# Performance work log

Hardware: AMD Instinct MI355X
Metric: run time of the kernel (lower is better)

Reference implementation:

```python
import jax, jax.numpy as jnp
import numpy as np

B, S, HID = 2, 4096, 2048
NH, NKV, HD = 32, 8, 64
GROUPS = NH // NKV
ROPE_THETA = 10000.0


def _rope_cos_sin(seq_len, dim, dtype):
    inv_freq = 1.0 / (ROPE_THETA ** (jnp.arange(0, dim, 2, dtype=jnp.float32) / dim))
    pos = jnp.arange(seq_len, dtype=jnp.float32)
    freqs = pos[:, None] * inv_freq[None, :]          # [S, D/2]
    emb = jnp.concatenate([freqs, freqs], axis=-1)    # [S, D]
    return jnp.cos(emb).astype(dtype), jnp.sin(emb).astype(dtype)


def _rotate_half(x):
    x1, x2 = jnp.split(x, 2, axis=-1)
    return jnp.concatenate([-x2, x1], axis=-1)


def _apply_rope(x, cos, sin):
    # x: [B, H, S, D]; cos/sin: [S, D]
    return x * cos[None, None] + _rotate_half(x) * sin[None, None]


def kappa(x):
    return jax.nn.elu(x) + 1.0


def setup_inputs() -> dict:
    key = jax.random.key(0)
    ks = jax.random.split(key, 6)
    sc = 0.02
    return {
        "hidden_states": jax.random.normal(ks[0], (B, S, HID), jnp.float32),
        "Wq": jax.random.normal(ks[1], (HID, NH * HD), jnp.float32) * sc,
        "Wk": jax.random.normal(ks[2], (HID, NKV * HD), jnp.float32) * sc,
        "Wv": jax.random.normal(ks[3], (HID, NKV * HD), jnp.float32) * sc,
        "Wphi": jax.random.normal(ks[4], (HID, HID), jnp.float32) * sc,
        "Wo": jax.random.normal(ks[5], (HID, HID), jnp.float32) * sc,
    }


def reference(hidden_states, Wq, Wk, Wv, Wphi, Wo):
    bsz, q_len, _ = hidden_states.shape

    q = (hidden_states @ Wq).reshape(bsz, q_len, NH, HD).transpose(0, 2, 1, 3)   # [B,NH,S,D]
    k = (hidden_states @ Wk).reshape(bsz, q_len, NKV, HD).transpose(0, 2, 1, 3)  # [B,NKV,S,D]
    v = (hidden_states @ Wv).reshape(bsz, q_len, NKV, HD).transpose(0, 2, 1, 3)

    cos, sin = _rope_cos_sin(q_len, HD, hidden_states.dtype)
    q = _apply_rope(q, cos, sin)
    k = _apply_rope(k, cos, sin)

    # repeat_kv for GQA: [B,NKV,S,D] -> [B,NH,S,D]
    k = jnp.repeat(k, GROUPS, axis=1)
    v = jnp.repeat(v, GROUPS, axis=1)

    Qk = kappa(q)   # [B,NH,S,D]
    Kk = kappa(k)

    Qg = Qk.mean(axis=2)                                # [B,NH,D] global query
    logits = jnp.einsum("bnd,bnsd->bns", Qg, Kk)        # [B,NH,S]
    alpha = jax.nn.softmax(logits, axis=-1) * float(q_len)

    # KV aggregation: [B,NH,D,D] state
    outer_sum = jnp.einsum("bns,bnsd,bnsf->bndf", alpha, Kk, v)
    result_attn = jnp.einsum("bnsd,bndf->bnsf", Qk, outer_sum)  # [B,NH,S,D]

    X_phi = (hidden_states @ Wphi).reshape(bsz, q_len, NH, HD).transpose(0, 2, 1, 3)
    ctx = (X_phi * result_attn).transpose(0, 2, 1, 3).reshape(bsz, q_len, HID)
    return ctx @ Wo
```

## Files before the change

### kernel.cpp

```cpp
#include <hip/hip_runtime.h>
#include <hip/hip_bf16.h>

#define B_ 2
#define S_ 4096
#define HID_ 2048
#define NH_ 32
#define NKV_ 8
#define HD_ 64
#define GROUPS_ 4
#define NCH_ 32
#define NLIN_ 5120

typedef short short8 __attribute__((ext_vector_type(8)));
typedef float floatx4 __attribute__((ext_vector_type(4)));

__device__ __forceinline__ float bf2f(unsigned short u){
  union { unsigned int i; float f; } v; v.i = ((unsigned int)u) << 16; return v.f;
}
__device__ __forceinline__ unsigned short f2bf(float f){
  union { float f; unsigned int i; } v; v.f = f;
  unsigned int i = v.i;
  unsigned int r = (i + 0x7fffu + ((i >> 16) & 1u)) >> 16;
  return (unsigned short)r;
}

__device__ __forceinline__ void async_copy16(unsigned short* lds, const unsigned short* g){
  __builtin_amdgcn_global_load_lds((const __attribute__((address_space(1))) void*)g,
                                   (__attribute__((address_space(3))) void*)lds,
                                   16, 0, 0);
}

__global__ void conv_bf16(const float* __restrict__ x, unsigned short* __restrict__ y, int n4){
  int i = blockIdx.x * 256 + threadIdx.x;
  if (i < n4){
    float4 v = ((const float4*)x)[i];
    ushort4 o;
    o.x = f2bf(v.x); o.y = f2bf(v.y); o.z = f2bf(v.z); o.w = f2bf(v.w);
    ((ushort4*)y)[i] = o;
  }
}

__global__ void transpose_all(const float* __restrict__ Wq, const float* __restrict__ Wk,
                              const float* __restrict__ Wv, const float* __restrict__ Wphi,
                              const float* __restrict__ Wo,
                              unsigned short* __restrict__ wcat, unsigned short* __restrict__ wot){
  const float* W; unsigned short* Wt; int N;
  switch (blockIdx.z){
    case 0:  W = Wq;   Wt = wcat;                              N = 2048; break;
    case 1:  W = Wk;   Wt = wcat + (size_t)2048 * HID_;        N = 512;  break;
    case 2:  W = Wv;   Wt = wcat + (size_t)2560 * HID_;        N = 512;  break;
    case 3:  W = Wphi; Wt = wcat + (size_t)3072 * HID_;        N = 2048; break;
    default: W = Wo;   Wt = wot;                               N = 2048; break;
  }
  int n0 = blockIdx.x * 32, k0 = blockIdx.y * 32;
  if (n0 >= N) return;
  __shared__ float tile[32][33];
  int tx = threadIdx.x, ty = threadIdx.y;
  #pragma unroll
  for (int j = 0; j < 4; j++)
    tile[ty + j*8][tx] = W[(size_t)(k0 + ty + j*8) * N + n0 + tx];
  __syncthreads();
  #pragma unroll
  for (int j = 0; j < 4; j++)
    Wt[(size_t)(n0 + ty + j*8) * HID_ + k0 + tx] = f2bf(tile[tx][ty + j*8]);
}

#define GTILE 16384

__global__ __launch_bounds__(512, 2) void gemm256(
    const unsigned short* __restrict__ A, const unsigned short* __restrict__ Bt,
    void* __restrict__ Cv, int M, int N, int K, int cbf16)
{
  __shared__ __align__(16) unsigned short As[2 * GTILE];
  __shared__ __align__(16) unsigned short Bs[2 * GTILE];

  const int tid = threadIdx.x;
  const int w = tid >> 6, lane = tid & 63;
  const int wr = w >> 2, wc = w & 3;
  const int l15 = lane & 15, quad = lane >> 4;

  const int nbx = N >> 8;
  int flat = blockIdx.y * nbx + blockIdx.x;
  int nwg  = nbx * (M >> 8);
  int cpx  = nwg >> 3;
  int swz  = (flat & 7) * cpx + (flat >> 3);
  int bx = swz % nbx, by = swz / nbx;
  const int m0 = by << 8, n0 = bx << 8;

  const int srow = (w << 3) + (lane >> 3);
  const int scc  = (lane & 7) ^ (lane >> 3);
  const unsigned short* gA = A  + (size_t)(m0 + srow) * K + scc * 8;
  const unsigned short* gB = Bt + (size_t)(n0 + srow) * K + scc * 8;
  const size_t rs64  = (size_t)64  * K;
  const size_t rs128 = (size_t)128 * K;
  unsigned short* lA0 = As + (w << 9);
  unsigned short* lB0 = Bs + (w << 9);

#define STAGE_A(bsel, h, t) do { \
    unsigned short* _d = lA0 + (bsel) * GTILE + (h) * 8192; \
    const unsigned short* _g = gA + (size_t)(h) * rs128 + (size_t)(t) * 64; \
    async_copy16(_d, _g); \
    async_copy16(_d + 4096, _g + rs64); \
  } while (0)
#define STAGE_B(bsel, h, t) do { \
    unsigned short* _d = lB0 + (bsel) * GTILE + (h) * 8192; \
    const unsigned short* _g = gB + (size_t)(h) * rs128 + (size_t)(t) * 64; \
    async_copy16(_d, _g); \
    async_copy16(_d + 4096, _g + rs64); \
  } while (0)
#define SCHED0 __builtin_amdgcn_sched_barrier(0)

  const int ks0  = ((quad     ^ (lane & 7)) << 3);
  const int ks1  = (((4+quad) ^ (lane & 7)) << 3);
  const int arow0 = (wr * 64 + l15) * 64;
  const int brow0 = (wc * 32 + l15) * 64;

  floatx4 acc[8][4] = {};
  short8 af[8][2], bfr[4][2];

  const int nt = K >> 6;

  STAGE_A(0, 0, 0); STAGE_A(0, 1, 0); STAGE_B(0, 0, 0); STAGE_B(0, 1, 0);
  if (nt > 1){
    STAGE_A(1, 0, 1); STAGE_B(1, 0, 1); STAGE_B(1, 1, 1);
    asm volatile("s_waitcnt vmcnt(6)" ::: "memory");
  } else {
    asm volatile("s_waitcnt vmcnt(0)" ::: "memory");
  }
  SCHED0;
  __builtin_amdgcn_s_barrier();
  SCHED0;

  for (int T = 0; T < nt; ++T){
    const int cb = T & 1;
    const unsigned short* Ab = As + cb * GTILE;
    const unsigned short* Bb = Bs + cb * GTILE;

    #pragma unroll
    for (int m = 0; m < 4; ++m){
      af[m][0] = *(const short8*)(Ab + arow0 + m * 1024 + ks0);
      af[m][1] = *(const short8*)(Ab + arow0 + m * 1024 + ks1);
    }
    #pragma unroll
    for (int n = 0; n < 2; ++n){
      bfr[n][0] = *(const short8*)(Bb + brow0 + n * 1024 + ks0);
      bfr[n][1] = *(const short8*)(Bb + brow0 + n * 1024 + ks1);
    }
    if (T + 1 < nt){ STAGE_A(cb ^ 1, 1, T + 1); }
    SCHED0; __builtin_amdgcn_s_barrier(); SCHED0;
    __builtin_amdgcn_s_setprio(1);
    #pragma unroll
    for (int k = 0; k < 2; ++k)
      #pragma unroll
      for (int m = 0; m < 4; ++m)
        #pragma unroll
        for (int n = 0; n < 2; ++n)
          acc[m][n] = __builtin_amdgcn_mfma_f32_16x16x32_bf16(af[m][k], bfr[n][k], acc[m][n], 0, 0, 0);
    __builtin_amdgcn_s_setprio(0);
    SCHED0; __builtin_amdgcn_s_barrier(); SCHED0;

    #pragma unroll
    for (int n = 2; n < 4; ++n){
      bfr[n][0] = *(const short8*)(Bb + brow0 + 8192 + (n - 2) * 1024 + ks0);
      bfr[n][1] = *(const short8*)(Bb + brow0 + 8192 + (n - 2) * 1024 + ks1);
    }
    if (T + 2 < nt){ STAGE_A(cb, 0, T + 2); }
    SCHED0; __builtin_amdgcn_s_barrier(); SCHED0;
    __builtin_amdgcn_s_setprio(1);
    #pragma unroll
    for (int k = 0; k < 2; ++k)
      #pragma unroll
      for (int m = 0; m < 4; ++m)
        #pragma unroll
        for (int n = 2; n < 4; ++n)
          acc[m][n] = __builtin_amdgcn_mfma_f32_16x16x32_bf16(af[m][k], bfr[n][k], acc[m][n], 0, 0, 0);
    __builtin_amdgcn_s_setprio(0);
    SCHED0; __builtin_amdgcn_s_barrier(); SCHED0;

    #pragma unroll
    for (int m = 4; m < 8; ++m){
      af[m][0] = *(const short8*)(Ab + arow0 + 8192 + (m - 4) * 1024 + ks0);
      af[m][1] = *(const short8*)(Ab + arow0 + 8192 + (m - 4) * 1024 + ks1);
    }
    if (T + 2 < nt){ STAGE_B(cb, 0, T + 2); }
    SCHED0; __builtin_amdgcn_s_barrier(); SCHED0;
    __builtin_amdgcn_s_setprio(1);
    #pragma unroll
    for (int k = 0; k < 2; ++k)
      #pragma unroll
      for (int m = 4; m < 8; ++m)
        #pragma unroll
        for (int n = 0; n < 2; ++n)
          acc[m][n] = __builtin_amdgcn_mfma_f32_16x16x32_bf16(af[m][k], bfr[n][k], acc[m][n], 0, 0, 0);
    __builtin_amdgcn_s_setprio(0);
    SCHED0; __builtin_amdgcn_s_barrier(); SCHED0;

    if (T + 2 < nt){
      STAGE_B(cb, 1, T + 2);
      asm volatile("s_waitcnt vmcnt(6)" ::: "memory");
    } else {
      asm volatile("s_waitcnt vmcnt(0)" ::: "memory");
    }
    SCHED0; __builtin_amdgcn_s_barrier(); SCHED0;
    __builtin_amdgcn_s_setprio(1);
    #pragma unroll
    for (int k = 0; k < 2; ++k)
      #pragma unroll
      for (int m = 4; m < 8; ++m)
        #pragma unroll
        for (int n = 2; n < 4; ++n)
          acc[m][n] = __builtin_amdgcn_mfma_f32_16x16x32_bf16(af[m][k], bfr[n][k], acc[m][n], 0, 0, 0);
    __builtin_amdgcn_s_setprio(0);
    SCHED0; __builtin_amdgcn_s_barrier(); SCHED0;
  }

#undef STAGE_A
#undef STAGE_B
#undef SCHED0

  if (cbf16){
    unsigned short* Cb = (unsigned short*)Cv;
    #pragma unroll
    for (int mi = 0; mi < 8; ++mi){
      const int row = m0 + (mi & 3) * 16 + wr * 64 + (mi >> 2) * 128 + quad * 4;
      #pragma unroll
      for (int ni = 0; ni < 4; ++ni){
        const int col = n0 + (ni & 1) * 16 + wc * 32 + (ni >> 1) * 128 + l15;
        #pragma unroll
        for (int r = 0; r < 4; ++r)
          Cb[(size_t)(row + r) * N + col] = f2bf(acc[mi][ni][r]);
      }
    }
  } else {
    float* Cf = (float*)Cv;
    #pragma unroll
    for (int mi = 0; mi < 8; ++mi){
      const int row = m0 + (mi & 3) * 16 + wr * 64 + (mi >> 2) * 128 + quad * 4;
      #pragma unroll
      for (int ni = 0; ni < 4; ++ni){
        const int col = n0 + (ni & 1) * 16 + wc * 32 + (ni >> 1) * 128 + l15;
        #pragma unroll
        for (int r = 0; r < 4; ++r)
          Cf[(size_t)(row + r) * N + col] = acc[mi][ni][r];
      }
    }
  }
}

__global__ void rope_fused(const unsigned short* __restrict__ lin,
                           unsigned short* __restrict__ Qk, unsigned short* __restrict__ Kk){
  int blk = blockIdx.x;
  if (blk < 32768){
    int idx = blk * 256 + threadIdx.x;
    int i = idx & 31;
    int n = (idx >> 5) & (NH_ - 1);
    int s = (idx >> 10) & (S_ - 1);
    int b = idx >> 22;
    float invf = exp2f(-(float)i * (13.287712379549449f / 32.0f));
    float ang = (float)s * invf;
    float c = cosf(ang), sn = sinf(ang);
    size_t in_o = (size_t)(b * S_ + s) * NLIN_ + n * HD_;
    float x1 = bf2f(lin[in_o + i]);
    float x2 = bf2f(lin[in_o + i + 32]);
    float r1 = x1 * c - x2 * sn;
    float r2 = x2 * c + x1 * sn;
    r1 = r1 > 0.f ? r1 + 1.f : __expf(r1);
    r2 = r2 > 0.f ? r2 + 1.f : __expf(r2);
    size_t o = ((size_t)(b * NH_ + n) * S_ + s) * HD_;
    Qk[o + i] = f2bf(r1);
    Qk[o + i + 32] = f2bf(r2);
  } else {
    int idx = (blk - 32768) * 256 + threadIdx.x;
    int i = idx & 31;
    int kv = (idx >> 5) & (NKV_ - 1);
    int s = (idx >> 8) & (S_ - 1);
    int b = idx >> 20;
    float invf = exp2f(-(float)i * (13.287712379549449f / 32.0f));
    float ang = (float)s * invf;
    float c = cosf(ang), sn = sinf(ang);
    size_t in_o = (size_t)(b * S_ + s) * NLIN_ + 2048 + kv * HD_;
    float x1 = bf2f(lin[in_o + i]);
    float x2 = bf2f(lin[in_o + i + 32]);
    float r1 = x1 * c - x2 * sn;
    float r2 = x2 * c + x1 * sn;
    r1 = r1 > 0.f ? r1 + 1.f : __expf(r1);
    r2 = r2 > 0.f ? r2 + 1.f : __expf(r2);
    size_t o = ((size_t)(b * NKV_ + kv) * S_ + s) * HD_;
    Kk[o + i] = f2bf(r1);
    Kk[o + i + 32] = f2bf(r2);
  }
}

__global__ __launch_bounds__(256) void qg_mean(const unsigned short* __restrict__ Qk,
                                               float* __restrict__ Qg){
  int bn = blockIdx.x, chunk = blockIdx.y;
  int tid = threadIdx.x;
  int dgrp = tid & 7, sgrp = tid >> 3;
  const unsigned short* base = Qk + (size_t)bn * S_ * HD_
                             + (size_t)(chunk * 256 + sgrp) * HD_ + dgrp * 8;
  float acc[8] = {};
  #pragma unroll
  for (int i = 0; i < 8; i++){
    short8 v = *(const short8*)(base + (size_t)i * 32 * HD_);
    #pragma unroll
    for (int e = 0; e < 8; e++) acc[e] += bf2f((unsigned short)v[e]);
  }
  __shared__ float red[256][8];
  #pragma unroll
  for (int e = 0; e < 8; e++) red[tid][e] = acc[e];
  __syncthreads();
  if (tid < 64){
    int dg = tid >> 3, e = tid & 7;
    float s = 0.f;
    #pragma unroll
    for (int g = 0; g < 32; g++) s += red[g * 8 + dg][e];
    atomicAdd(&Qg[bn * 64 + tid], s * (1.0f / (float)S_));
  }
}

__global__ __launch_bounds__(256) void logits_kernel(const unsigned short* __restrict__ Kk,
                                                     const float* __restrict__ Qg,
                                                     float* __restrict__ logits){
  int bn = blockIdx.x, chunk = blockIdx.y;
  int b = bn / NH_, n = bn % NH_, kv = n / GROUPS_;
  int tid = threadIdx.x;
  __shared__ float qg[64];
  if (tid < 64) qg[tid] = Qg[bn * 64 + tid];
  __syncthreads();
  int s = chunk * 256 + tid;
  const unsigned short* row = Kk + ((size_t)(b * NKV_ + kv) * S_ + s) * HD_;
  float acc = 0.f;
  #pragma unroll
  for (int c = 0; c < 8; c++){
    short8 v = *(const short8*)(row + c * 8);
    #pragma unroll
    for (int e = 0; e < 8; e++) acc += qg[c * 8 + e] * bf2f((unsigned short)v[e]);
  }
  logits[(size_t)bn * S_ + s] = acc;
}

__global__ __launch_bounds__(256) void softmax_kernel(const float* __restrict__ logits,
                                                      float* __restrict__ alpha){
  int bn = blockIdx.x;
  int tid = threadIdx.x;
  float l[16];
  float mymax = -1e30f;
  #pragma unroll
  for (int j = 0; j < 16; j++){
    l[j] = logits[(size_t)bn * S_ + j * 256 + tid];
    mymax = fmaxf(mymax, l[j]);
  }
  __shared__ float red[256];
  red[tid] = mymax; __syncthreads();
  for (int st = 128; st > 0; st >>= 1){
    if (tid < st) red[tid] = fmaxf(red[tid], red[tid + st]);
    __syncthreads();
  }
  float gmax = red[0];
  __syncthreads();
  float mysum = 0.f;
  #pragma unroll
  for (int j = 0; j < 16; j++){ l[j] = __expf(l[j] - gmax); mysum += l[j]; }
  red[tid] = mysum; __syncthreads();
  for (int st = 128; st > 0; st >>= 1){
    if (tid < st) red[tid] += red[tid + st];
    __syncthreads();
  }
  float inv = (float)S_ / red[0];
  #pragma unroll
  for (int j = 0; j < 16; j++)
    alpha[(size_t)bn * S_ + j * 256 + tid] = l[j] * inv;
}

__global__ __launch_bounds__(256) void outer_sum_kernel(const unsigned short* __restrict__ Kk,
                                                        const unsigned short* __restrict__ lin,
                                                        const float* __restrict__ alpha,
                                                        float* __restrict__ part){
  int bkv = blockIdx.x, chunk = blockIdx.y;
  int b = bkv >> 3, kv = bkv & 7;
  int tid = threadIdx.x;
  int d = tid >> 2, fb = (tid & 3) * 16;
  __shared__ float ks[64][64];
  __shared__ float vs[64][64];
  __shared__ float as4[64][4];
  float acc[4][16] = {};
  const unsigned short* kb = Kk + (size_t)(b * NKV_ + kv) * S_ * HD_;
  const int SPC = S_ / NCH_;

  for (int t = 0; t < SPC / 64; t++){
    int ss = chunk * SPC + t * 64;
    #pragma unroll
    for (int jj = 0; jj < 4; jj++){
      int idx4 = jj * 256 + tid;
      int si = idx4 >> 4, c4 = (idx4 & 15) * 4;
      ushort4 kv4 = *(const ushort4*)(kb + (size_t)(ss + si) * HD_ + c4);
      ks[si][c4]   = bf2f(kv4.x); ks[si][c4+1] = bf2f(kv4.y);
      ks[si][c4+2] = bf2f(kv4.z); ks[si][c4+3] = bf2f(kv4.w);
      ushort4 vv4 = *(const ushort4*)(lin + (size_t)(b * S_ + ss + si) * NLIN_ + 2560 + kv * HD_ + c4);
      vs[si][c4]   = bf2f(vv4.x); vs[si][c4+1] = bf2f(vv4.y);
      vs[si][c4+2] = bf2f(vv4.z); vs[si][c4+3] = bf2f(vv4.w);
    }
    {
      int si = tid >> 2, h = tid & 3;
      as4[si][h] = alpha[(size_t)(b * NH_ + kv * GROUPS_ + h) * S_ + ss + si];
    }
    __syncthreads();
    #pragma unroll 4
    for (int si = 0; si < 64; si++){
      float k = ks[si][d];
      float4 a4 = *(const float4*)&as4[si][0];
      float4 v0 = *(const float4*)&vs[si][fb];
      float4 v1 = *(const float4*)&vs[si][fb + 4];
      float4 v2 = *(const float4*)&vs[si][fb + 8];
      float4 v3 = *(const float4*)&vs[si][fb + 12];
      float ak0 = a4.x * k, ak1 = a4.y * k, ak2 = a4.z * k, ak3 = a4.w * k;
      acc[0][0]  += ak0 * v0.x; acc[0][1]  += ak0 * v0.y; acc[0][2]  += ak0 * v0.z; acc[0][3]  += ak0 * v0.w;
      acc[0][4]  += ak0 * v1.x; acc[0][5]  += ak0 * v1.y; acc[0][6]  += ak0 * v1.z; acc[0][7]  += ak0 * v1.w;
      acc[0][8]  += ak0 * v2.x; acc[0][9]  += ak0 * v2.y; acc[0][10] += ak0 * v2.z; acc[0][11] += ak0 * v2.w;
      acc[0][12] += ak0 * v3.x; acc[0][13] += ak0 * v3.y; acc[0][14] += ak0 * v3.z; acc[0][15] += ak0 * v3.w;
      acc[1][0]  += ak1 * v0.x; acc[1][1]  += ak1 * v0.y; acc[1][2]  += ak1 * v0.z; acc[1][3]  += ak1 * v0.w;
      acc[1][4]  += ak1 * v1.x; acc[1][5]  += ak1 * v1.y; acc[1][6]  += ak1 * v1.z; acc[1][7]  += ak1 * v1.w;
      acc[1][8]  += ak1 * v2.x; acc[1][9]  += ak1 * v2.y; acc[1][10] += ak1 * v2.z; acc[1][11] += ak1 * v2.w;
      acc[1][12] += ak1 * v3.x; acc[1][13] += ak1 * v3.y; acc[1][14] += ak1 * v3.z; acc[1][15] += ak1 * v3.w;
      acc[2][0]  += ak2 * v0.x; acc[2][1]  += ak2 * v0.y; acc[2][2]  += ak2 * v0.z; acc[2][3]  += ak2 * v0.w;
      acc[2][4]  += ak2 * v1.x; acc[2][5]  += ak2 * v1.y; acc[2][6]  += ak2 * v1.z; acc[2][7]  += ak2 * v1.w;
      acc[2][8]  += ak2 * v2.x; acc[2][9]  += ak2 * v2.y; acc[2][10] += ak2 * v2.z; acc[2][11] += ak2 * v2.w;
      acc[2][12] += ak2 * v3.x; acc[2][13] += ak2 * v3.y; acc[2][14] += ak2 * v3.z; acc[2][15] += ak2 * v3.w;
      acc[3][0]  += ak3 * v0.x; acc[3][1]  += ak3 * v0.y; acc[3][2]  += ak3 * v0.z; acc[3][3]  += ak3 * v0.w;
      acc[3][4]  += ak3 * v1.x; acc[3][5]  += ak3 * v1.y; acc[3][6]  += ak3 * v1.z; acc[3][7]  += ak3 * v1.w;
      acc[3][8]  += ak3 * v2.x; acc[3][9]  += ak3 * v2.y; acc[3][10] += ak3 * v2.z; acc[3][11] += ak3 * v2.w;
      acc[3][12] += ak3 * v3.x; acc[3][13] += ak3 * v3.y; acc[3][14] += ak3 * v3.z; acc[3][15] += ak3 * v3.w;
    }
    __syncthreads();
  }

  #pragma unroll
  for (int h = 0; h < 4; h++){
    float* pb = part + ((size_t)(chunk * 16 + bkv) * 4 + h) * 4096 + d * 64 + fb;
    #pragma unroll
    for (int j = 0; j < 4; j++)
      *(float4*)&pb[j * 4] = *(float4*)&acc[h][j * 4];
  }
}

__global__ __launch_bounds__(256) void osum_reduce_t(const float* __restrict__ part,
                                                     unsigned short* __restrict__ osumb){
  int bn = blockIdx.x;
  int tid = threadIdx.x;
  __shared__ float os[64][65];
  const float4* p4 = (const float4*)part;
  #pragma unroll
  for (int r = 0; r < 4; r++){
    int idx4 = r * 256 + tid;
    float4 s = {0.f, 0.f, 0.f, 0.f};
    #pragma unroll 8
    for (int c = 0; c < NCH_; c++){
      float4 v = p4[(size_t)c * 65536 + bn * 1024 + idx4];
      s.x += v.x; s.y += v.y; s.z += v.z; s.w += v.w;
    }
    int d = idx4 >> 4;
    int f0 = (idx4 & 15) * 4;
    os[d][f0] = s.x; os[d][f0+1] = s.y; os[d][f0+2] = s.z; os[d][f0+3] = s.w;
  }
  __syncthreads();
  int f = tid >> 2, d0 = (tid & 3) * 16;
  unsigned short hi[16], lo[16];
  #pragma unroll
  for (int j = 0; j < 16; j++){
    float x = os[d0 + j][f];
    unsigned short h = f2bf(x);
    hi[j] = h;
    lo[j] = f2bf(x - bf2f(h));
  }
  unsigned short* oh = osumb + ((size_t)bn * 2) * 4096 + (size_t)f * 64 + d0;
  unsigned short* ol = oh + 4096;
  *(short8*)(oh)     = *(const short8*)(hi);
  *(short8*)(oh + 8) = *(const short8*)(hi + 8);
  *(short8*)(ol)     = *(const short8*)(lo);
  *(short8*)(ol + 8) = *(const short8*)(lo + 8);
}

__global__ __launch_bounds__(256) void ctx_mfma(const unsigned short* __restrict__ Qk,
                                                const unsigned short* __restrict__ osumb,
                                                const unsigned short* __restrict__ lin,
                                                unsigned short* __restrict__ ctx){
  int bn = blockIdx.x, sc = blockIdx.y;
  int b = bn >> 5, n = bn & 31;
  int tid = threadIdx.x;
  int w = tid >> 6, lane = tid & 63;
  int l15 = lane & 15, quad = lane >> 4;

  const unsigned short* obase = osumb + ((size_t)bn * 2) * 4096;
  short8 bh[4][2], bl[4][2];
  #pragma unroll
  for (int nf = 0; nf < 4; nf++){
    int f = nf * 16 + l15;
    #pragma unroll
    for (int kh = 0; kh < 2; kh++){
      bh[nf][kh] = *(const short8*)(obase + (size_t)f * 64 + kh * 32 + quad * 8);
      bl[nf][kh] = *(const short8*)(obase + 4096 + (size_t)f * 64 + kh * 32 + quad * 8);
    }
  }

  int s0 = sc * 256 + w * 64;
  const unsigned short* qbase = Qk + ((size_t)bn * S_ + s0) * HD_;
  floatx4 acc[4][4] = {};
  #pragma unroll
  for (int m = 0; m < 4; m++){
    short8 a0 = *(const short8*)(qbase + (size_t)(m * 16 + l15) * HD_ + quad * 8);
    short8 a1 = *(const short8*)(qbase + (size_t)(m * 16 + l15) * HD_ + 32 + quad * 8);
    #pragma unroll
    for (int nf = 0; nf < 4; nf++){
      acc[m][nf] = __builtin_amdgcn_mfma_f32_16x16x32_bf16(a0, bh[nf][0], acc[m][nf], 0, 0, 0);
      acc[m][nf] = __builtin_amdgcn_mfma_f32_16x16x32_bf16(a1, bh[nf][1], acc[m][nf], 0, 0, 0);
      acc[m][nf] = __builtin_amdgcn_mfma_f32_16x16x32_bf16(a0, bl[nf][0], acc[m][nf], 0, 0, 0);
      acc[m][nf] = __builtin_amdgcn_mfma_f32_16x16x32_bf16(a1, bl[nf][1], acc[m][nf], 0, 0, 0);
    }
  }

  #pragma unroll
  for (int m = 0; m < 4; m++){
    #pragma unroll
    for (int r = 0; r < 4; r++){
      int s = s0 + m * 16 + quad * 4 + r;
      const unsigned short* xp = lin + (size_t)(b * S_ + s) * NLIN_ + 3072 + n * HD_;
      unsigned short* cp = ctx + (size_t)(b * S_ + s) * HID_ + n * HD_;
      #pragma unroll
      for (int nf = 0; nf < 4; nf++){
        int f = nf * 16 + l15;
        cp[f] = f2bf(bf2f(xp[f]) * acc[m][nf][r]);
      }
    }
  }
}

extern "C" void kernel_launch(void* const* d_in, const int* in_sizes, int n_in,
                              void* d_out, int out_size, void* d_ws, size_t ws_size,
                              hipStream_t stream) {
  const float* hs   = (const float*)d_in[0];
  const float* Wq   = (const float*)d_in[1];
  const float* Wk   = (const float*)d_in[2];
  const float* Wv   = (const float*)d_in[3];
  const float* Wphi = (const float*)d_in[4];
  const float* Wo   = (const float*)d_in[5];
  float* out = (float*)d_out;

  char* ws = (char*)d_ws;
  const size_t M = (size_t)B_ * S_;
  size_t off = 0;
  auto alloc = [&](size_t bytes){ size_t o = off; off += (bytes + 255) & ~(size_t)255; return o; };

  size_t off_x     = alloc(M * HID_ * 4);
  size_t off_wcat  = alloc((size_t)NLIN_ * HID_ * 2);
  size_t off_wot   = alloc((size_t)HID_ * HID_ * 2);
  size_t off_lin   = alloc(M * NLIN_ * 2);
  size_t off_qk    = alloc(M * HID_ * 2);
  size_t off_kk    = alloc(M * 512 * 2);
  size_t off_qg    = alloc(64 * 64 * 4);
  size_t off_alph  = alloc((size_t)B_ * NH_ * S_ * 4);
  size_t off_osumb = alloc((size_t)64 * 2 * 4096 * 2);
  (void)ws_size;

  unsigned short* hsb  = (unsigned short*)(ws + off_x);
  float*          part = (float*)(ws + off_x);
  unsigned short* ctx  = (unsigned short*)(ws + off_x);
  unsigned short* wcat = (unsigned short*)(ws + off_wcat);
  unsigned short* wot  = (unsigned short*)(ws + off_wot);
  unsigned short* lin  = (unsigned short*)(ws + off_lin);
  unsigned short* qk = (unsigned short*)(ws + off_qk);
  unsigned short* kk = (unsigned short*)(ws + off_kk);
  float* qg   = (float*)(ws + off_qg);
  float* alph = (float*)(ws + off_alph);
  unsigned short* osumb = (unsigned short*)(ws + off_osumb);

  conv_bf16<<<(int)(M * HID_ / 4 / 256), 256, 0, stream>>>(hs, hsb, (int)(M * HID_ / 4));
  transpose_all<<<dim3(64, 64, 5), dim3(32, 8), 0, stream>>>(Wq, Wk, Wv, Wphi, Wo, wcat, wot);
  gemm256<<<dim3(NLIN_/256, M/256), 512, 0, stream>>>(hsb, wcat, lin, (int)M, NLIN_, HID_, 1);
  rope_fused<<<32768 + 8192, 256, 0, stream>>>(lin, qk, kk);
  hipMemsetAsync(qg, 0, 64 * 64 * 4, stream);
  qg_mean<<<dim3(B_ * NH_, S_ / 256), 256, 0, stream>>>(qk, qg);
  logits_kernel<<<dim3(B_ * NH_, S_ / 256), 256, 0, stream>>>(kk, qg, alph);
  softmax_kernel<<<B_ * NH_, 256, 0, stream>>>(alph, alph);
  outer_sum_kernel<<<dim3(B_ * NKV_, NCH_), 256, 0, stream>>>(kk, lin, alph, part);
  osum_reduce_t<<<64, 256, 0, stream>>>(part, osumb);
  ctx_mfma<<<dim3(B_ * NH_, S_ / 64 / 4), 256, 0, stream>>>(qk, osumb, lin, ctx);
  gemm256<<<dim3(HID_/256, M/256), 512, 0, stream>>>(ctx, wot, out, (int)M, HID_, HID_, 0);
}
```

Before: 516.6 us.

## Fuse query mean into RoPE kernel and stage ctx epilogue through shared memory

The RoPE/kappa kernel now accumulates the per-head query mean while writing Qk, which removes the separate qg_mean pass that re-read all of Qk. Each block handles 256 sequence positions per head and uses fast __sincosf. The ctx_mfma epilogue writes accumulators to LDS as bf16, then performs coalesced 16-byte loads of X_phi and 16-byte stores of ctx in place of scattered 2-byte accesses. The risks are fewer, longer-running blocks in the RoPE kernel (1280 blocks in place of about 41k), an extra bf16 rounding of the attention result before the multiply, and the lower accuracy of __sincosf at large angles.

Measured after the change: 515.5 us. Within noise of the previous version (-0.2%).

```diff
diff --git a/kernel.cpp b/kernel.cpp
--- a/kernel.cpp
+++ b/kernel.cpp
@@ -247,74 +247,60 @@
   }
 }
 
-__global__ void rope_fused(const unsigned short* __restrict__ lin,
-                           unsigned short* __restrict__ Qk, unsigned short* __restrict__ Kk){
-  int blk = blockIdx.x;
-  if (blk < 32768){
-    int idx = blk * 256 + threadIdx.x;
-    int i = idx & 31;
-    int n = (idx >> 5) & (NH_ - 1);
-    int s = (idx >> 10) & (S_ - 1);
-    int b = idx >> 22;
-    float invf = exp2f(-(float)i * (13.287712379549449f / 32.0f));
-    float ang = (float)s * invf;
-    float c = cosf(ang), sn = sinf(ang);
-    size_t in_o = (size_t)(b * S_ + s) * NLIN_ + n * HD_;
-    float x1 = bf2f(lin[in_o + i]);
-    float x2 = bf2f(lin[in_o + i + 32]);
-    float r1 = x1 * c - x2 * sn;
-    float r2 = x2 * c + x1 * sn;
-    r1 = r1 > 0.f ? r1 + 1.f : __expf(r1);
-    r2 = r2 > 0.f ? r2 + 1.f : __expf(r2);
-    size_t o = ((size_t)(b * NH_ + n) * S_ + s) * HD_;
-    Qk[o + i] = f2bf(r1);
-    Qk[o + i + 32] = f2bf(r2);
+__global__ __launch_bounds__(256) void rope_fused(const unsigned short* __restrict__ lin,
+                                                  unsigned short* __restrict__ Qk,
+                                                  unsigned short* __restrict__ Kk,
+                                                  float* __restrict__ Qg){
+  int bx = blockIdx.x, sc = blockIdx.y;
+  int tid = threadIdx.x;
+  int i = tid & 31, si = tid >> 5;
+  float invf = exp2f(-(float)i * (13.287712379549449f / 32.0f));
+  if (bx < 64){
+    int bn = bx, b = bx >> 5, n = bx & 31;
+    float qa0 = 0.f, qa1 = 0.f;
+    for (int j = 0; j < 32; ++j){
+      int s = sc * 256 + j * 8 + si;
+      size_t in_o = (size_t)(b * S_ + s) * NLIN_ + n * HD_;
+      float x1 = bf2f(lin[in_o + i]);
+      float x2 = bf2f(lin[in_o + i + 32]);
+      float sn, c;
+      __sincosf((float)s * invf, &sn, &c);
+      float r1 = x1 * c - x2 * sn;
+      float r2 = x2 * c + x1 * sn;
+      r1 = r1 > 0.f ? r1 + 1.f : __expf(r1);
+      r2 = r2 > 0.f ? r2 + 1.f : __expf(r2);
+      size_t o = ((size_t)bn * S_ + s) * HD_;
+      Qk[o + i] = f2bf(r1);
+      Qk[o + i + 32] = f2bf(r2);
+      qa0 += r1; qa1 += r2;
+    }
+    __shared__ float red[8][64];
+    red[si][i] = qa0;
+    red[si][i + 32] = qa1;
+    __syncthreads();
+    if (tid < 64){
+      float ssum = 0.f;
+      #pragma unroll
+      for (int g = 0; g < 8; ++g) ssum += red[g][tid];
+      atomicAdd(&Qg[bn * 64 + tid], ssum * (1.0f / (float)S_));
+    }
   } else {
-    int idx = (blk - 32768) * 256 + threadIdx.x;
-    int i = idx & 31;
-    int kv = (idx >> 5) & (NKV_ - 1);
-    int s = (idx >> 8) & (S_ - 1);
-    int b = idx >> 20;
-    float invf = exp2f(-(float)i * (13.287712379549449f / 32.0f));
-    float ang = (float)s * invf;
-    float c = cosf(ang), sn = sinf(ang);
-    size_t in_o = (size_t)(b * S_ + s) * NLIN_ + 2048 + kv * HD_;
-    float x1 = bf2f(lin[in_o + i]);
-    float x2 = bf2f(lin[in_o + i + 32]);
-    float r1 = x1 * c - x2 * sn;
-    float r2 = x2 * c + x1 * sn;
-    r1 = r1 > 0.f ? r1 + 1.f : __expf(r1);
-    r2 = r2 > 0.f ? r2 + 1.f : __expf(r2);
-    size_t o = ((size_t)(b * NKV_ + kv) * S_ + s) * HD_;
-    Kk[o + i] = f2bf(r1);
-    Kk[o + i + 32] = f2bf(r2);
-  }
-}
-
-__global__ __launch_bounds__(256) void qg_mean(const unsigned short* __restrict__ Qk,
-                                               float* __restrict__ Qg){
-  int bn = blockIdx.x, chunk = blockIdx.y;
-  int tid = threadIdx.x;
-  int dgrp = tid & 7, sgrp = tid >> 3;
-  const unsigned short* base = Qk + (size_t)bn * S_ * HD_
-                             + (size_t)(chunk * 256 + sgrp) * HD_ + dgrp * 8;
-  float acc[8] = {};
-  #pragma unroll
-  for (int i = 0; i < 8; i++){
-    short8 v = *(const short8*)(base + (size_t)i * 32 * HD_);
-    #pragma unroll
-    for (int e = 0; e < 8; e++) acc[e] += bf2f((unsigned short)v[e]);
-  }
-  __shared__ float red[256][8];
-  #pragma unroll
-  for (int e = 0; e < 8; e++) red[tid][e] = acc[e];
-  __syncthreads();
-  if (tid < 64){
-    int dg = tid >> 3, e = tid & 7;
-    float s = 0.f;
-    #pragma unroll
-    for (int g = 0; g < 32; g++) s += red[g * 8 + dg][e];
-    atomicAdd(&Qg[bn * 64 + tid], s * (1.0f / (float)S_));
+    int bkv = bx - 64, b = bkv >> 3, kv = bkv & 7;
+    for (int j = 0; j < 32; ++j){
+      int s = sc * 256 + j * 8 + si;
+      size_t in_o = (size_t)(b * S_ + s) * NLIN_ + 2048 + kv * HD_;
+      float x1 = bf2f(lin[in_o + i]);
+      float x2 = bf2f(lin[in_o + i + 32]);
+      float sn, c;
+      __sincosf((float)s * invf, &sn, &c);
+      float r1 = x1 * c - x2 * sn;
+      float r2 = x2 * c + x1 * sn;
+      r1 = r1 > 0.f ? r1 + 1.f : __expf(r1);
+      r2 = r2 > 0.f ? r2 + 1.f : __expf(r2);
+      size_t o = ((size_t)(b * NKV_ + kv) * S_ + s) * HD_;
+      Kk[o + i] = f2bf(r1);
+      Kk[o + i + 32] = f2bf(r2);
+    }
   }
 }
 
@@ -490,6 +476,8 @@
   int w = tid >> 6, lane = tid & 63;
   int l15 = lane & 15, quad = lane >> 4;
 
+  __shared__ unsigned short rb[256][72];
+
   const unsigned short* obase = osumb + ((size_t)bn * 2) * 4096;
   short8 bh[4][2], bl[4][2];
   #pragma unroll
@@ -519,18 +507,27 @@
   }
 
   #pragma unroll
-  for (int m = 0; m < 4; m++){
-    #pragma unroll
-    for (int r = 0; r < 4; r++){
-      int s = s0 + m * 16 + quad * 4 + r;
-      const unsigned short* xp = lin + (size_t)(b * S_ + s) * NLIN_ + 3072 + n * HD_;
-      unsigned short* cp = ctx + (size_t)(b * S_ + s) * HID_ + n * HD_;
-      #pragma unroll
-      for (int nf = 0; nf < 4; nf++){
-        int f = nf * 16 + l15;
-        cp[f] = f2bf(bf2f(xp[f]) * acc[m][nf][r]);
-      }
-    }
+  for (int m = 0; m < 4; m++)
+    #pragma unroll
+    for (int nf = 0; nf < 4; nf++)
+      #pragma unroll
+      for (int r = 0; r < 4; r++)
+        rb[w * 64 + m * 16 + quad * 4 + r][nf * 16 + l15] = f2bf(acc[m][nf][r]);
+  __syncthreads();
+
+  int srow = tid;
+  int s = sc * 256 + srow;
+  const unsigned short* xp = lin + (size_t)(b * S_ + s) * NLIN_ + 3072 + n * HD_;
+  unsigned short* cp = ctx + (size_t)(b * S_ + s) * HID_ + n * HD_;
+  #pragma unroll
+  for (int c = 0; c < 8; c++){
+    short8 xv = *(const short8*)(xp + c * 8);
+    short8 rv = *(const short8*)(&rb[srow][c * 8]);
+    unsigned short o8[8];
+    #pragma unroll
+    for (int e = 0; e < 8; e++)
+      o8[e] = f2bf(bf2f((unsigned short)xv[e]) * bf2f((unsigned short)rv[e]));
+    *(short8*)(cp + c * 8) = *(const short8*)o8;
   }
 }
 
@@ -576,9 +573,8 @@
   conv_bf16<<<(int)(M * HID_ / 4 / 256), 256, 0, stream>>>(hs, hsb, (int)(M * HID_ / 4));
   transpose_all<<<dim3(64, 64, 5), dim3(32, 8), 0, stream>>>(Wq, Wk, Wv, Wphi, Wo, wcat, wot);
   gemm256<<<dim3(NLIN_/256, M/256), 512, 0, stream>>>(hsb, wcat, lin, (int)M, NLIN_, HID_, 1);
-  rope_fused<<<32768 + 8192, 256, 0, stream>>>(lin, qk, kk);
   hipMemsetAsync(qg, 0, 64 * 64 * 4, stream);
-  qg_mean<<<dim3(B_ * NH_, S_ / 256), 256, 0, stream>>>(qk, qg);
+  rope_fused<<<dim3(80, 16), 256, 0, stream>>>(lin, qk, kk, qg);
   logits_kernel<<<dim3(B_ * NH_, S_ / 256), 256, 0, stream>>>(kk, qg, alph);
   softmax_kernel<<<B_ * NH_, 256, 0, stream>>>(alph, alph);
   outer_sum_kernel<<<dim3(B_ * NKV_, NCH_), 256, 0, stream>>>(kk, lin, alph, part);
```
